# Kernel optimization log

Measured on AMD Instinct MI355X. Metric: run time of the kernel, lower is better.

Reference implementation:

```python
import jax, jax.numpy as jnp
import numpy as np

B, N, H, E, L = 64, 100, 128, 128, 3  # batch, nodes, node_hidden, edge_hidden, gcn layers


def setup_inputs() -> dict:
    key = jax.random.key(0)
    ks = jax.random.split(key, 12)
    s = 0.05
    return dict(
        node=jax.random.normal(ks[0], (B, N, 2), jnp.float32),
        demand=jax.random.uniform(ks[1], (B, N), jnp.float32),
        dis=jax.random.uniform(ks[2], (B, N, N), jnp.float32),
        Wn0=jax.random.normal(ks[3], (3, H), jnp.float32) * s,
        bn0=jnp.zeros((H,), jnp.float32),
        Ws=jax.random.normal(ks[4], (L, H, H), jnp.float32) * s,
        Wngh=jax.random.normal(ks[5], (L, H, H), jnp.float32) * s,
        We=jax.random.normal(ks[6], (E,), jnp.float32) * s,
        be=jnp.zeros((E,), jnp.float32),
        Wih=jax.random.normal(ks[7], (2, H, 3 * H), jnp.float32) * s,
        Whh=jax.random.normal(ks[8], (2, H, 3 * H), jnp.float32) * s,
        bih=jnp.zeros((2, 3 * H), jnp.float32),
        bhh=jnp.zeros((2, 3 * H), jnp.float32),
        Wq=jax.random.normal(ks[9], (H, H), jnp.float32) * s,
        Wc=jax.random.normal(ks[10], (E, 2), jnp.float32) * s,
        bc=jnp.zeros((2,), jnp.float32),
    )


def _gru(xin, h, Wih, Whh, bih, bhh):
    gi = xin @ Wih + bih
    gh = h @ Whh + bhh
    ir, iz, inn = jnp.split(gi, 3, -1)
    hr, hz, hn = jnp.split(gh, 3, -1)
    r = jax.nn.sigmoid(ir + hr)
    z = jax.nn.sigmoid(iz + hz)
    n = jnp.tanh(inn + r * hn)
    return (1.0 - z) * n + z * h


def _decode(x, Wih, Whh, bih, bhh, Wq, sample, key):
    b, n, h = x.shape
    scale = 1.0 / np.sqrt(h).astype(np.float32)

    def step(carry, _):
        last, hid, k = carry
        emb = x[jnp.arange(b), last]                      # [b,h]
        h0 = _gru(emb, hid[0], Wih[0], Whh[0], bih[0], bhh[0])
        h1 = _gru(h0, hid[1], Wih[1], Whh[1], bih[1], bhh[1])
        logits = jnp.einsum('bh,bnh->bn', h1 @ Wq, x) * scale
        logp = jax.nn.log_softmax(logits, -1)
        k, sk = jax.random.split(k)
        if sample:
            ind = jax.random.categorical(sk, logits)
        else:
            ind = jnp.argmax(logits, -1)
        ind = ind.astype(jnp.int32)
        chosen = jnp.take_along_axis(logp, ind[:, None], 1)[:, 0]
        return (ind, jnp.stack([h0, h1]), k), (ind, chosen)

    init = (jnp.zeros((b,), jnp.int32), jnp.zeros((2, b, h), x.dtype), key)
    _, (inds, lps) = jax.lax.scan(step, init, None, length=n - 1)
    solution = jnp.concatenate([jnp.zeros((b, 1), jnp.int32), inds.T], axis=1)  # depot 0 first
    return lps.T, solution  # logprob [b,n-1], solution [b,n]


def _count_dist(sol, dis):
    bidx = jnp.arange(sol.shape[0])[:, None]
    return dis[bidx, sol[:, :-1], sol[:, 1:]].sum(axis=1, keepdims=True)  # [b,1]


def reference(node, demand, dis, Wn0, bn0, Ws, Wngh, We, be, Wih, Whh, bih, bhh, Wq, Wc, bc):
    # --- GCN encoder ---
    h = jax.nn.relu(jnp.concatenate([node, demand[..., None]], -1) @ Wn0 + bn0)  # [B,N,H]
    A = jax.nn.softmax(-dis, -1)  # distance-based soft adjacency
    for l in range(Ws.shape[0]):
        h = jax.nn.relu(h @ Ws[l] + jnp.einsum('bij,bjh->bih', A, h @ Wngh[l]))
    e = jax.nn.relu(dis[..., None] * We + be)  # [B,N,N,E]

    key = jax.random.key(42)
    k1, _ = jax.random.split(key)
    sample_logprob, sample_solution = _decode(h, Wih, Whh, bih, bhh, Wq, True, k1)
    sample_distance = _count_dist(sample_solution, dis)
    _, greedy_solution = _decode(h, Wih, Whh, bih, bhh, Wq, False, k1)
    greedy_distance = _count_dist(greedy_solution, dis)

    predict_matrix = jax.nn.softmax(e @ Wc + bc, -1)  # [B,N,N,2]

    b, n = h.shape[0], h.shape[1]
    bidx = jnp.arange(b)[:, None]
    greedy_solution_matrix = (
        jnp.zeros((b, n, n), jnp.int32)
        .at[bidx, greedy_solution[:, :-1], greedy_solution[:, 1:]]
        .set(1)
    )
    return (sample_logprob, sample_distance, greedy_distance, predict_matrix, greedy_solution_matrix)
```

## Files before the change

### kernel.cpp

```cpp
#include <hip/hip_runtime.h>
#include <math.h>

#define BB 64
#define NN 100
#define HH 128
#define T3 384

#define O0 0
#define O1 6336
#define O2 6400
#define O3 6464
#define O4 1286464

#define TINYF 1.17549435e-38f
#define SCALEF 0.08838834764831845f

__device__ __forceinline__ unsigned rotl32(unsigned x, int d) {
    return (x << d) | (x >> (32 - d));
}

__device__ __forceinline__ void tf2x32(unsigned ks0, unsigned ks1,
                                       unsigned x0, unsigned x1,
                                       unsigned& o0, unsigned& o1) {
    unsigned ks2 = ks0 ^ ks1 ^ 0x1BD11BDAu;
    x0 += ks0; x1 += ks1;
    x0 += x1; x1 = rotl32(x1, 13); x1 ^= x0;
    x0 += x1; x1 = rotl32(x1, 15); x1 ^= x0;
    x0 += x1; x1 = rotl32(x1, 26); x1 ^= x0;
    x0 += x1; x1 = rotl32(x1, 6);  x1 ^= x0;
    x0 += ks1; x1 += ks2 + 1u;
    x0 += x1; x1 = rotl32(x1, 17); x1 ^= x0;
    x0 += x1; x1 = rotl32(x1, 29); x1 ^= x0;
    x0 += x1; x1 = rotl32(x1, 16); x1 ^= x0;
    x0 += x1; x1 = rotl32(x1, 24); x1 ^= x0;
    x0 += ks2; x1 += ks0 + 2u;
    x0 += x1; x1 = rotl32(x1, 13); x1 ^= x0;
    x0 += x1; x1 = rotl32(x1, 15); x1 ^= x0;
    x0 += x1; x1 = rotl32(x1, 26); x1 ^= x0;
    x0 += x1; x1 = rotl32(x1, 6);  x1 ^= x0;
    x0 += ks0; x1 += ks1 + 3u;
    x0 += x1; x1 = rotl32(x1, 17); x1 ^= x0;
    x0 += x1; x1 = rotl32(x1, 29); x1 ^= x0;
    x0 += x1; x1 = rotl32(x1, 16); x1 ^= x0;
    x0 += x1; x1 = rotl32(x1, 24); x1 ^= x0;
    x0 += ks1; x1 += ks2 + 4u;
    x0 += x1; x1 = rotl32(x1, 13); x1 ^= x0;
    x0 += x1; x1 = rotl32(x1, 15); x1 ^= x0;
    x0 += x1; x1 = rotl32(x1, 26); x1 ^= x0;
    x0 += x1; x1 = rotl32(x1, 6);  x1 ^= x0;
    x0 += ks2; x1 += ks0 + 5u;
    o0 = x0; o1 = x1;
}

__device__ __forceinline__ float gumbel_f(unsigned k0, unsigned k1, unsigned f) {
    unsigned o0, o1;
    tf2x32(k0, k1, 0u, f, o0, o1);
    unsigned bits = o0 ^ o1;
    float u01 = __uint_as_float((bits >> 9) | 0x3F800000u) - 1.0f;
    float u = fmaxf(TINYF, u01 * (1.0f - TINYF) + TINYF);
    return -logf(-logf(u));
}

__global__ void k_embed_adj(const float* __restrict__ node, const float* __restrict__ demand,
                            const float* __restrict__ Wn0, const float* __restrict__ bn0,
                            const float* __restrict__ dis,
                            float* __restrict__ h, float* __restrict__ A) {
    int bid = blockIdx.x, tid = threadIdx.x;
    if (bid < 3200) {
        int idx = bid * 256 + tid;
        int r = idx >> 7, c = idx & 127;
        float v = node[r * 2] * Wn0[c] + node[r * 2 + 1] * Wn0[128 + c]
                + demand[r] * Wn0[256 + c] + bn0[c];
        h[idx] = fmaxf(v, 0.0f);
    } else {
        int row = (bid - 3200) * 4 + (tid >> 6);
        int l = tid & 63;
        const float* d = dis + row * NN;
        float v0 = -d[l];
        float v1 = (l + 64 < NN) ? -d[l + 64] : -__builtin_inff();
        float m = fmaxf(v0, v1);
        for (int off = 32; off > 0; off >>= 1) m = fmaxf(m, __shfl_xor(m, off));
        float e0 = expf(v0 - m);
        float e1 = (l + 64 < NN) ? expf(v1 - m) : 0.0f;
        float s = e0 + e1;
        for (int off = 32; off > 0; off >>= 1) s += __shfl_xor(s, off);
        float inv = 1.0f / s;
        A[row * NN + l] = e0 * inv;
        if (l + 64 < NN) A[row * NN + l + 64] = e1 * inv;
    }
}

__global__ void k_hw16(const float* __restrict__ h, const float* __restrict__ W,
                       float* __restrict__ out) {
    __shared__ float hs[16 * 128];
    int block_row = blockIdx.x * 16;
    int tid = threadIdx.x;
    int col = tid & 127;
    int rg = tid >> 7;
    for (int i = tid; i < 16 * 128; i += 256) hs[i] = h[block_row * 128 + i];
    __syncthreads();
    float acc[8] = {0.f, 0.f, 0.f, 0.f, 0.f, 0.f, 0.f, 0.f};
    for (int k = 0; k < 128; k++) {
        float w = W[k * 128 + col];
#pragma unroll
        for (int r = 0; r < 8; r++) acc[r] += hs[(rg + 2 * r) * 128 + k] * w;
    }
#pragma unroll
    for (int r = 0; r < 8; r++)
        out[(block_row + rg + 2 * r) * 128 + col] = acc[r];
}

__global__ void k_zp(const float* __restrict__ h, const float* __restrict__ WqT,
                     const float* __restrict__ Wih, const float* __restrict__ bih,
                     float* __restrict__ Z, float* __restrict__ P0) {
    __shared__ float hs[16 * 128];
    int block_row = blockIdx.x * 16;
    int tid = threadIdx.x;
    int c = tid & 127;
    int rg = tid >> 7;
    int y = blockIdx.y;
    for (int i = tid; i < 16 * 128; i += 256) hs[i] = h[block_row * 128 + i];
    __syncthreads();
    float acc[8] = {0.f, 0.f, 0.f, 0.f, 0.f, 0.f, 0.f, 0.f};
    if (y == 0) {
        for (int k = 0; k < 128; k++) {
            float w = WqT[k * 128 + c];
#pragma unroll
            for (int r = 0; r < 8; r++) acc[r] += hs[(rg + 2 * r) * 128 + k] * w;
        }
#pragma unroll
        for (int r = 0; r < 8; r++)
            Z[(block_row + rg + 2 * r) * 128 + c] = acc[r];
    } else {
        int col = (y - 1) * 128 + c;
        for (int k = 0; k < 128; k++) {
            float w = Wih[k * 384 + col];
#pragma unroll
            for (int r = 0; r < 8; r++) acc[r] += hs[(rg + 2 * r) * 128 + k] * w;
        }
        float bb = bih[col];
#pragma unroll
        for (int r = 0; r < 8; r++)
            P0[(size_t)(block_row + rg + 2 * r) * 384 + col] = acc[r] + bb;
    }
}

__global__ void k_transpose128(const float* __restrict__ Wq, float* __restrict__ WqT) {
    int i = blockIdx.x * 256 + threadIdx.x;
    if (i >= 128 * 128) return;
    int k = i >> 7, c = i & 127;
    WqT[k * 128 + c] = Wq[c * 128 + k];
}

__global__ void k_agg10(const float* __restrict__ h, const float* __restrict__ Ws,
                        const float* __restrict__ A, const float* __restrict__ hw,
                        float* __restrict__ out) {
    __shared__ float hs[10 * 128];
    __shared__ float As[10 * 100];
    int b = blockIdx.x / 10;
    int i0 = (blockIdx.x % 10) * 10;
    int tid = threadIdx.x;
    int col = tid & 127;
    int rg = tid >> 7;
    int rowbase = b * NN + i0;
    for (int i = tid; i < 10 * 128; i += 256) hs[i] = h[rowbase * 128 + i];
    for (int i = tid; i < 10 * 100; i += 256) As[i] = A[rowbase * 100 + i];
    __syncthreads();
    float acc[5] = {0.f, 0.f, 0.f, 0.f, 0.f};
    for (int k = 0; k < 128; k++) {
        float w = Ws[k * 128 + col];
#pragma unroll
        for (int r = 0; r < 5; r++) acc[r] += hs[(rg + 2 * r) * 128 + k] * w;
    }
    const float* hwb = hw + b * NN * 128;
    for (int j = 0; j < NN; j++) {
        float v = hwb[j * 128 + col];
#pragma unroll
        for (int r = 0; r < 5; r++) acc[r] += As[(rg + 2 * r) * 100 + j] * v;
    }
#pragma unroll
    for (int r = 0; r < 5; r++)
        out[(rowbase + rg + 2 * r) * 128 + col] = fmaxf(acc[r], 0.0f);
}

__global__ void k_predict_zero(const float* __restrict__ dis, const float* __restrict__ We,
                               const float* __restrict__ be, const float* __restrict__ Wc,
                               const float* __restrict__ bc, float* __restrict__ out3,
                               float* __restrict__ zp) {
    int bid = blockIdx.x, tid = threadIdx.x;
    if (bid >= 1250) {
        int i = (bid - 1250) * 256 + tid;
        float4 z; z.x = 0.f; z.y = 0.f; z.z = 0.f; z.w = 0.f;
        ((float4*)zp)[i] = z;
        return;
    }
    __shared__ float sWe[128], sbe[128], sc0[128], sc1[128];
    if (tid < 128) {
        sWe[tid] = We[tid];
        sbe[tid] = be[tid];
        sc0[tid] = Wc[tid * 2];
        sc1[tid] = Wc[tid * 2 + 1];
    }
    __syncthreads();
    float b0 = bc[0], b1 = bc[1];
    int p0 = bid * 512 + tid, p1 = p0 + 256;
    float d0 = dis[p0], d1 = dis[p1];
    float a00 = b0, a01 = b1, a10 = b0, a11 = b1;
    for (int k = 0; k < 128; k++) {
        float we = sWe[k], bbe = sbe[k], c0 = sc0[k], c1 = sc1[k];
        float e0 = fmaxf(d0 * we + bbe, 0.0f);
        float e1 = fmaxf(d1 * we + bbe, 0.0f);
        a00 += e0 * c0; a01 += e0 * c1;
        a10 += e1 * c0; a11 += e1 * c1;
    }
    {
        float m = fmaxf(a00, a01);
        float q0 = expf(a00 - m), q1 = expf(a01 - m);
        float inv = 1.0f / (q0 + q1);
        out3[p0 * 2] = q0 * inv;
        out3[p0 * 2 + 1] = q1 * inv;
    }
    {
        float m = fmaxf(a10, a11);
        float q0 = expf(a10 - m), q1 = expf(a11 - m);
        float inv = 1.0f / (q0 + q1);
        out3[p1 * 2] = q0 * inv;
        out3[p1 * 2 + 1] = q1 * inv;
    }
}

__device__ __forceinline__ void matvec_tile4(const float* __restrict__ W,
                                             const float* __restrict__ hp,
                                             int nk4,
                                             float* __restrict__ pg0,
                                             float* __restrict__ pg1) {
    float a00 = 0.f, a01 = 0.f, a02 = 0.f, a03 = 0.f;
    float a10 = 0.f, a11 = 0.f, a12 = 0.f, a13 = 0.f;
#pragma unroll 4
    for (int k4 = 0; k4 < nk4; ++k4) {
        float4 hA = *(const float4*)(hp + 4 * k4);
        float4 hB = *(const float4*)(hp + 132 + 4 * k4);
        const float* Wk = W + (size_t)(4 * k4) * T3;
        float4 w0 = *(const float4*)(Wk);
        float4 w1 = *(const float4*)(Wk + T3);
        float4 w2 = *(const float4*)(Wk + 2 * T3);
        float4 w3 = *(const float4*)(Wk + 3 * T3);
        a00 += hA.x * w0.x; a01 += hA.x * w0.y; a02 += hA.x * w0.z; a03 += hA.x * w0.w;
        a10 += hB.x * w0.x; a11 += hB.x * w0.y; a12 += hB.x * w0.z; a13 += hB.x * w0.w;
        a00 += hA.y * w1.x; a01 += hA.y * w1.y; a02 += hA.y * w1.z; a03 += hA.y * w1.w;
        a10 += hB.y * w1.x; a11 += hB.y * w1.y; a12 += hB.y * w1.z; a13 += hB.y * w1.w;
        a00 += hA.z * w2.x; a01 += hA.z * w2.y; a02 += hA.z * w2.z; a03 += hA.z * w2.w;
        a10 += hB.z * w2.x; a11 += hB.z * w2.y; a12 += hB.z * w2.z; a13 += hB.z * w2.w;
        a00 += hA.w * w3.x; a01 += hA.w * w3.y; a02 += hA.w * w3.z; a03 += hA.w * w3.w;
        a10 += hB.w * w3.x; a11 += hB.w * w3.y; a12 += hB.w * w3.z; a13 += hB.w * w3.w;
    }
    float4 o;
    o.x = a00; o.y = a01; o.z = a02; o.w = a03;
    *(float4*)pg0 = o;
    o.x = a10; o.y = a11; o.z = a12; o.w = a13;
    *(float4*)pg1 = o;
}

__global__ __launch_bounds__(768, 3) void k_decode9(
    const float* __restrict__ P0,
    const float* __restrict__ Z,
    const float* __restrict__ dis,
    const float* __restrict__ Wih,
    const float* __restrict__ Whh,
    const float* __restrict__ bih,
    const float* __restrict__ bhh,
    float* __restrict__ out) {
    __shared__ float Zs[NN * 132];
    __shared__ float h0s[2 * 132], h1s[2 * 132];
    __shared__ float pgA[4 * 2 * 392];
    __shared__ float pgB[4 * 2 * 392];
    __shared__ float pgC[8 * 2 * 392];
    __shared__ float sbhh0[T3], sbih1[T3], sbhh1[T3];
    __shared__ float pl[2 * 2 * 100];
    __shared__ float gum[128];
    __shared__ int s_ind2[2];

    const int tid = threadIdx.x;
    const int b = blockIdx.x;

    const float* __restrict__ Wih1 = Wih + 128 * T3;

    for (int i4 = tid; i4 < NN * 32; i4 += 768) {
        int r = i4 >> 5, c4 = (i4 & 31) * 4;
        *(float4*)&Zs[r * 132 + c4] = *(const float4*)&Z[(b * NN + r) * 128 + c4];
    }
    if (tid < T3) {
        sbhh0[tid] = bhh[tid];
        sbih1[tid] = bih[T3 + tid];
        sbhh1[tid] = bhh[T3 + tid];
    }
    if (tid < 256) {
        int m = tid >> 7, i = tid & 127;
        h0s[m * 132 + i] = 0.0f;
        h1s[m * 132 + i] = 0.0f;
    }
    if (tid == 0) { s_ind2[0] = 0; s_ind2[1] = 0; }

    unsigned kk0, kk1;
    tf2x32(0u, 42u, 0u, 0u, kk0, kk1);

    const int unitA = tid / 384;
    const int rA = tid - unitA * 384;
    const int ksA = rA / 96, j4A = rA - ksA * 96;
    const int j0A = j4A * 4, k0A = ksA * 32;
    const int ksC = tid / 96, j4C = tid - ksC * 96;
    const int j0C = j4C * 4, k0C = ksC * 16;

    int lastm = 0;
    float dist = 0.0f;
    __syncthreads();

    for (int t = 0; t < NN - 1; t++) {
        unsigned sk0, sk1, nkA, nkB;
        tf2x32(kk0, kk1, 0u, 1u, sk0, sk1);
        tf2x32(kk0, kk1, 0u, 0u, nkA, nkB);
        kk0 = nkA; kk1 = nkB;

        float pf_r = 0.f, pf_z = 0.f, pf_n = 0.f;
        if (tid < 256) {
            const float* P0row = P0 + (size_t)(b * NN + s_ind2[tid >> 7]) * T3;
            int i = tid & 127;
            pf_r = P0row[i];
            pf_z = P0row[i + 128];
            pf_n = P0row[i + 256];
        }

        {
            const float* W = Whh + unitA * (128 * T3) + (size_t)k0A * T3 + j0A;
            const float* hp = ((unitA == 0) ? h0s : h1s) + k0A;
            float* pg = (unitA == 0) ? pgA : pgB;
            matvec_tile4(W, hp, 8,
                         &pg[(ksA * 2 + 0) * 392 + j0A],
                         &pg[(ksA * 2 + 1) * 392 + j0A]);
        }
        __syncthreads();

        if (tid < 256) {
            int m = tid >> 7, i = tid & 127;
            float ghr = sbhh0[i], ghz = sbhh0[i + 128], ghn = sbhh0[i + 256];
#pragma unroll
            for (int ks = 0; ks < 4; ks++) {
                int pb = (ks * 2 + m) * 392;
                ghr += pgA[pb + i];
                ghz += pgA[pb + i + 128];
                ghn += pgA[pb + i + 256];
            }
            float rr = 1.0f / (1.0f + expf(-(pf_r + ghr)));
            float zz = 1.0f / (1.0f + expf(-(pf_z + ghz)));
            float nn = tanhf(pf_n + rr * ghn);
            h0s[m * 132 + i] = (1.0f - zz) * nn + zz * h0s[m * 132 + i];
        } else if (tid < 356) {
            int u = tid - 256;
            gum[u] = gumbel_f(sk0, sk1, (unsigned)(b * NN + u));
        }
        __syncthreads();

        {
            const float* W = Wih1 + (size_t)k0C * T3 + j0C;
            matvec_tile4(W, h0s + k0C, 4,
                         &pgC[(ksC * 2 + 0) * 392 + j0C],
                         &pgC[(ksC * 2 + 1) * 392 + j0C]);
        }
        __syncthreads();

        if (tid < 256) {
            int m = tid >> 7, i = tid & 127;
            float gir = sbih1[i], giz = sbih1[i + 128], gin = sbih1[i + 256];
#pragma unroll
            for (int ks = 0; ks < 8; ks++) {
                int pb = (ks * 2 + m) * 392;
                gir += pgC[pb + i];
                giz += pgC[pb + i + 128];
                gin += pgC[pb + i + 256];
            }
            float ghr = sbhh1[i], ghz = sbhh1[i + 128], ghn = sbhh1[i + 256];
#pragma unroll
            for (int ks = 0; ks < 4; ks++) {
                int pb = (ks * 2 + m) * 392;
                ghr += pgB[pb + i];
                ghz += pgB[pb + i + 128];
                ghn += pgB[pb + i + 256];
            }
            float rr = 1.0f / (1.0f + expf(-(gir + ghr)));
            float zz = 1.0f / (1.0f + expf(-(giz + ghz)));
            float nn = tanhf(gin + rr * ghn);
            h1s[m * 132 + i] = (1.0f - zz) * nn + zz * h1s[m * 132 + i];
        }
        __syncthreads();

        if (tid < 200) {
            int ks = tid / 100, n = tid - ks * 100;
            int kk0p = ks * 64;
            const float* Zp = &Zs[n * 132 + kk0p];
            const float* hp = &h1s[kk0p];
            float a0 = 0.f, a1 = 0.f;
#pragma unroll 4
            for (int q = 0; q < 16; q++) {
                float4 z4 = *(const float4*)(Zp + 4 * q);
                float4 hA = *(const float4*)(hp + 4 * q);
                float4 hB = *(const float4*)(hp + 132 + 4 * q);
                a0 += hA.x * z4.x; a0 += hA.y * z4.y; a0 += hA.z * z4.z; a0 += hA.w * z4.w;
                a1 += hB.x * z4.x; a1 += hB.y * z4.y; a1 += hB.z * z4.z; a1 += hB.w * z4.w;
            }
            pl[(0 * 2 + ks) * 100 + n] = a0;
            pl[(1 * 2 + ks) * 100 + n] = a1;
        }
        __syncthreads();

        if (tid < 128) {
            const int m = tid >> 6, lane = tid & 63;
            float v0, v1 = -__builtin_inff();
            v0 = (pl[(m * 2 + 0) * 100 + lane] + pl[(m * 2 + 1) * 100 + lane]) * SCALEF;
            if (lane + 64 < NN)
                v1 = (pl[(m * 2 + 0) * 100 + lane + 64] + pl[(m * 2 + 1) * 100 + lane + 64]) * SCALEF;
            float mx = fmaxf(v0, v1);
            for (int off = 32; off > 0; off >>= 1) mx = fmaxf(mx, __shfl_xor(mx, off));
            float e = expf(v0 - mx) + ((lane + 64 < NN) ? expf(v1 - mx) : 0.0f);
            for (int off = 32; off > 0; off >>= 1) e += __shfl_xor(e, off);
            float a0 = v0, a1 = v1;
            if (m == 0) {
                a0 += gum[lane];
                if (lane + 64 < NN) a1 += gum[lane + 64];
            }
            float bv; int bi;
            if (a1 > a0) { bv = a1; bi = lane + 64; } else { bv = a0; bi = lane; }
            for (int off = 32; off > 0; off >>= 1) {
                float ov = __shfl_xor(bv, off);
                int   oi = __shfl_xor(bi, off);
                if (ov > bv || (ov == bv && oi < bi)) { bv = ov; bi = oi; }
            }
            int ind = bi;
            float la = __shfl(v0, ind & 63);
            float lb = __shfl(v1, ind & 63);
            float lv = (ind < 64) ? la : lb;
            if (lane == 0) {
                if (m == 0) out[O0 + b * (NN - 1) + t] = lv - mx - logf(e);
                else        out[O4 + (size_t)b * NN * NN + lastm * NN + ind] = 1.0f;
                s_ind2[m] = ind;
            }
            dist += dis[b * NN * NN + lastm * NN + ind];
            lastm = ind;
        }
        __syncthreads();
    }

    if (tid == 0)  out[O1 + b] = dist;
    if (tid == 64) out[O2 + b] = dist;
}

extern "C" void kernel_launch(void* const* d_in, const int* in_sizes, int n_in,
                              void* d_out, int out_size, void* d_ws, size_t ws_size,
                              hipStream_t stream) {
    (void)in_sizes; (void)n_in; (void)out_size; (void)ws_size;
    const float* node   = (const float*)d_in[0];
    const float* demand = (const float*)d_in[1];
    const float* dis    = (const float*)d_in[2];
    const float* Wn0    = (const float*)d_in[3];
    const float* bn0    = (const float*)d_in[4];
    const float* Ws     = (const float*)d_in[5];
    const float* Wngh   = (const float*)d_in[6];
    const float* We     = (const float*)d_in[7];
    const float* be     = (const float*)d_in[8];
    const float* Wih    = (const float*)d_in[9];
    const float* Whh    = (const float*)d_in[10];
    const float* bih    = (const float*)d_in[11];
    const float* bhh    = (const float*)d_in[12];
    const float* Wq     = (const float*)d_in[13];
    const float* Wc     = (const float*)d_in[14];
    const float* bc     = (const float*)d_in[15];
    float* out = (float*)d_out;
    float* ws  = (float*)d_ws;

    float* hA  = ws;
    float* hB  = ws + 819200;
    float* hw  = ws + 1638400;
    float* A   = ws + 2457600;
    float* P0  = ws + 2457600;
    float* WqT = ws + 4915200;

    hipLaunchKernelGGL(k_predict_zero, dim3(1875), dim3(256), 0, stream,
                       dis, We, be, Wc, bc, out + O3, out + O4);

    hipLaunchKernelGGL(k_embed_adj, dim3(4800), dim3(256), 0, stream,
                       node, demand, Wn0, bn0, dis, hA, A);

    float* cur = hA;
    float* nxt = hB;
    for (int l = 0; l < 3; l++) {
        hipLaunchKernelGGL(k_hw16, dim3(400), dim3(256), 0, stream, cur, Wngh + l * 16384, hw);
        hipLaunchKernelGGL(k_agg10, dim3(640), dim3(256), 0, stream, cur, Ws + l * 16384, A, hw, nxt);
        float* tswap = cur; cur = nxt; nxt = tswap;
    }

    hipLaunchKernelGGL(k_transpose128, dim3(64), dim3(256), 0, stream, Wq, WqT);
    hipLaunchKernelGGL(k_zp, dim3(400, 4), dim3(256), 0, stream, cur, WqT, Wih, bih, hw, P0);

    hipLaunchKernelGGL(k_decode9, dim3(64), dim3(768), 0, stream,
                       P0, hw, dis, Wih, Whh, bih, bhh, out);
}
```

Baseline: 923.4 us.

## Cache decode GRU input weights in registers, merge preprocessing kernels, vectorize loads

Each decode thread now loads its 16x4 tile of the second-layer GRU input weights into registers once, instead of re-reading it from global memory on every sequential decode step. The predict, zero-fill, embed, adjacency-softmax and Wq transpose kernels are merged into one launch. The small GEMM-like kernels use float4 shared-memory staging and a 4-way unrolled k loop. The extra 64 live floats per thread under a 768-thread, 3-block launch bound may exceed the register budget and spill to scratch.

```diff
diff --git a/kernel.cpp b/kernel.cpp
--- a/kernel.cpp
+++ b/kernel.cpp
@@ -61,10 +61,16 @@
     return -logf(-logf(u));
 }
 
-__global__ void k_embed_adj(const float* __restrict__ node, const float* __restrict__ demand,
-                            const float* __restrict__ Wn0, const float* __restrict__ bn0,
-                            const float* __restrict__ dis,
-                            float* __restrict__ h, float* __restrict__ A) {
+__global__ void k_pre0(const float* __restrict__ node, const float* __restrict__ demand,
+                       const float* __restrict__ Wn0, const float* __restrict__ bn0,
+                       const float* __restrict__ dis,
+                       const float* __restrict__ We, const float* __restrict__ be,
+                       const float* __restrict__ Wc, const float* __restrict__ bc,
+                       const float* __restrict__ Wq,
+                       float* __restrict__ h, float* __restrict__ A,
+                       float* __restrict__ WqT,
+                       float* __restrict__ out3, float* __restrict__ zp) {
+    __shared__ float sWe[128], sbe[128], sc0[128], sc1[128];
     int bid = blockIdx.x, tid = threadIdx.x;
     if (bid < 3200) {
         int idx = bid * 256 + tid;
@@ -72,7 +78,7 @@
         float v = node[r * 2] * Wn0[c] + node[r * 2 + 1] * Wn0[128 + c]
                 + demand[r] * Wn0[256 + c] + bn0[c];
         h[idx] = fmaxf(v, 0.0f);
-    } else {
+    } else if (bid < 4800) {
         int row = (bid - 3200) * 4 + (tid >> 6);
         int l = tid & 63;
         const float* d = dis + row * NN;
@@ -87,6 +93,55 @@
         float inv = 1.0f / s;
         A[row * NN + l] = e0 * inv;
         if (l + 64 < NN) A[row * NN + l + 64] = e1 * inv;
+    } else if (bid < 4864) {
+        int i = (bid - 4800) * 256 + tid;
+        int k = i >> 7, c = i & 127;
+        WqT[k * 128 + c] = Wq[c * 128 + k];
+    } else if (bid < 6114) {
+        if (tid < 128) {
+            sWe[tid] = We[tid];
+            sbe[tid] = be[tid];
+            sc0[tid] = Wc[tid * 2];
+            sc1[tid] = Wc[tid * 2 + 1];
+        }
+        __syncthreads();
+        float b0 = bc[0], b1 = bc[1];
+        int p0 = (bid - 4864) * 512 + tid, p1 = p0 + 256;
+        float d0 = dis[p0], d1 = dis[p1];
+        float a00 = b0, a01 = b1, a10 = b0, a11 = b1;
+        for (int k4 = 0; k4 < 32; k4++) {
+            float4 we = *(const float4*)&sWe[4 * k4];
+            float4 bb = *(const float4*)&sbe[4 * k4];
+            float4 c0 = *(const float4*)&sc0[4 * k4];
+            float4 c1 = *(const float4*)&sc1[4 * k4];
+            float e0, e1;
+            e0 = fmaxf(d0 * we.x + bb.x, 0.0f); a00 += e0 * c0.x; a01 += e0 * c1.x;
+            e1 = fmaxf(d1 * we.x + bb.x, 0.0f); a10 += e1 * c0.x; a11 += e1 * c1.x;
+            e0 = fmaxf(d0 * we.y + bb.y, 0.0f); a00 += e0 * c0.y; a01 += e0 * c1.y;
+            e1 = fmaxf(d1 * we.y + bb.y, 0.0f); a10 += e1 * c0.y; a11 += e1 * c1.y;
+            e0 = fmaxf(d0 * we.z + bb.z, 0.0f); a00 += e0 * c0.z; a01 += e0 * c1.z;
+            e1 = fmaxf(d1 * we.z + bb.z, 0.0f); a10 += e1 * c0.z; a11 += e1 * c1.z;
+            e0 = fmaxf(d0 * we.w + bb.w, 0.0f); a00 += e0 * c0.w; a01 += e0 * c1.w;
+            e1 = fmaxf(d1 * we.w + bb.w, 0.0f); a10 += e1 * c0.w; a11 += e1 * c1.w;
+        }
+        {
+            float m = fmaxf(a00, a01);
+            float q0 = expf(a00 - m), q1 = expf(a01 - m);
+            float inv = 1.0f / (q0 + q1);
+            out3[p0 * 2] = q0 * inv;
+            out3[p0 * 2 + 1] = q1 * inv;
+        }
+        {
+            float m = fmaxf(a10, a11);
+            float q0 = expf(a10 - m), q1 = expf(a11 - m);
+            float inv = 1.0f / (q0 + q1);
+            out3[p1 * 2] = q0 * inv;
+            out3[p1 * 2 + 1] = q1 * inv;
+        }
+    } else {
+        int i = (bid - 6114) * 256 + tid;
+        float4 z; z.x = 0.f; z.y = 0.f; z.z = 0.f; z.w = 0.f;
+        ((float4*)zp)[i] = z;
     }
 }
 
@@ -97,13 +152,20 @@
     int tid = threadIdx.x;
     int col = tid & 127;
     int rg = tid >> 7;
-    for (int i = tid; i < 16 * 128; i += 256) hs[i] = h[block_row * 128 + i];
+    for (int i = tid; i < 16 * 32; i += 256)
+        ((float4*)hs)[i] = ((const float4*)(h + block_row * 128))[i];
     __syncthreads();
     float acc[8] = {0.f, 0.f, 0.f, 0.f, 0.f, 0.f, 0.f, 0.f};
-    for (int k = 0; k < 128; k++) {
-        float w = W[k * 128 + col];
-#pragma unroll
-        for (int r = 0; r < 8; r++) acc[r] += hs[(rg + 2 * r) * 128 + k] * w;
+    for (int k4 = 0; k4 < 32; k4++) {
+        int k = 4 * k4;
+        float w0 = W[k * 128 + col], w1 = W[(k + 1) * 128 + col];
+        float w2 = W[(k + 2) * 128 + col], w3 = W[(k + 3) * 128 + col];
+#pragma unroll
+        for (int r = 0; r < 8; r++) {
+            float4 h4 = *(const float4*)&hs[(rg + 2 * r) * 128 + k];
+            acc[r] += h4.x * w0; acc[r] += h4.y * w1;
+            acc[r] += h4.z * w2; acc[r] += h4.w * w3;
+        }
     }
 #pragma unroll
     for (int r = 0; r < 8; r++)
@@ -119,37 +181,43 @@
     int c = tid & 127;
     int rg = tid >> 7;
     int y = blockIdx.y;
-    for (int i = tid; i < 16 * 128; i += 256) hs[i] = h[block_row * 128 + i];
+    for (int i = tid; i < 16 * 32; i += 256)
+        ((float4*)hs)[i] = ((const float4*)(h + block_row * 128))[i];
     __syncthreads();
     float acc[8] = {0.f, 0.f, 0.f, 0.f, 0.f, 0.f, 0.f, 0.f};
     if (y == 0) {
-        for (int k = 0; k < 128; k++) {
-            float w = WqT[k * 128 + c];
-#pragma unroll
-            for (int r = 0; r < 8; r++) acc[r] += hs[(rg + 2 * r) * 128 + k] * w;
+        for (int k4 = 0; k4 < 32; k4++) {
+            int k = 4 * k4;
+            float w0 = WqT[k * 128 + c], w1 = WqT[(k + 1) * 128 + c];
+            float w2 = WqT[(k + 2) * 128 + c], w3 = WqT[(k + 3) * 128 + c];
+#pragma unroll
+            for (int r = 0; r < 8; r++) {
+                float4 h4 = *(const float4*)&hs[(rg + 2 * r) * 128 + k];
+                acc[r] += h4.x * w0; acc[r] += h4.y * w1;
+                acc[r] += h4.z * w2; acc[r] += h4.w * w3;
+            }
         }
 #pragma unroll
         for (int r = 0; r < 8; r++)
             Z[(block_row + rg + 2 * r) * 128 + c] = acc[r];
     } else {
         int col = (y - 1) * 128 + c;
-        for (int k = 0; k < 128; k++) {
-            float w = Wih[k * 384 + col];
-#pragma unroll
-            for (int r = 0; r < 8; r++) acc[r] += hs[(rg + 2 * r) * 128 + k] * w;
+        for (int k4 = 0; k4 < 32; k4++) {
+            int k = 4 * k4;
+            float w0 = Wih[k * 384 + col], w1 = Wih[(k + 1) * 384 + col];
+            float w2 = Wih[(k + 2) * 384 + col], w3 = Wih[(k + 3) * 384 + col];
+#pragma unroll
+            for (int r = 0; r < 8; r++) {
+                float4 h4 = *(const float4*)&hs[(rg + 2 * r) * 128 + k];
+                acc[r] += h4.x * w0; acc[r] += h4.y * w1;
+                acc[r] += h4.z * w2; acc[r] += h4.w * w3;
+            }
         }
         float bb = bih[col];
 #pragma unroll
         for (int r = 0; r < 8; r++)
             P0[(size_t)(block_row + rg + 2 * r) * 384 + col] = acc[r] + bb;
     }
-}
-
-__global__ void k_transpose128(const float* __restrict__ Wq, float* __restrict__ WqT) {
-    int i = blockIdx.x * 256 + threadIdx.x;
-    if (i >= 128 * 128) return;
-    int k = i >> 7, c = i & 127;
-    WqT[k * 128 + c] = Wq[c * 128 + k];
 }
 
 __global__ void k_agg10(const float* __restrict__ h, const float* __restrict__ Ws,
@@ -163,70 +231,38 @@
     int col = tid & 127;
     int rg = tid >> 7;
     int rowbase = b * NN + i0;
-    for (int i = tid; i < 10 * 128; i += 256) hs[i] = h[rowbase * 128 + i];
-    for (int i = tid; i < 10 * 100; i += 256) As[i] = A[rowbase * 100 + i];
+    for (int i = tid; i < 10 * 32; i += 256)
+        ((float4*)hs)[i] = ((const float4*)(h + rowbase * 128))[i];
+    for (int i = tid; i < 10 * 25; i += 256)
+        ((float4*)As)[i] = ((const float4*)(A + rowbase * 100))[i];
     __syncthreads();
     float acc[5] = {0.f, 0.f, 0.f, 0.f, 0.f};
-    for (int k = 0; k < 128; k++) {
-        float w = Ws[k * 128 + col];
-#pragma unroll
-        for (int r = 0; r < 5; r++) acc[r] += hs[(rg + 2 * r) * 128 + k] * w;
+    for (int k4 = 0; k4 < 32; k4++) {
+        int k = 4 * k4;
+        float w0 = Ws[k * 128 + col], w1 = Ws[(k + 1) * 128 + col];
+        float w2 = Ws[(k + 2) * 128 + col], w3 = Ws[(k + 3) * 128 + col];
+#pragma unroll
+        for (int r = 0; r < 5; r++) {
+            float4 h4 = *(const float4*)&hs[(rg + 2 * r) * 128 + k];
+            acc[r] += h4.x * w0; acc[r] += h4.y * w1;
+            acc[r] += h4.z * w2; acc[r] += h4.w * w3;
+        }
     }
     const float* hwb = hw + b * NN * 128;
-    for (int j = 0; j < NN; j++) {
-        float v = hwb[j * 128 + col];
-#pragma unroll
-        for (int r = 0; r < 5; r++) acc[r] += As[(rg + 2 * r) * 100 + j] * v;
+    for (int j4 = 0; j4 < 25; j4++) {
+        int j = 4 * j4;
+        float v0 = hwb[j * 128 + col], v1 = hwb[(j + 1) * 128 + col];
+        float v2 = hwb[(j + 2) * 128 + col], v3 = hwb[(j + 3) * 128 + col];
+#pragma unroll
+        for (int r = 0; r < 5; r++) {
+            float4 a4 = *(const float4*)&As[(rg + 2 * r) * 100 + j];
+            acc[r] += a4.x * v0; acc[r] += a4.y * v1;
+            acc[r] += a4.z * v2; acc[r] += a4.w * v3;
+        }
     }
 #pragma unroll
     for (int r = 0; r < 5; r++)
         out[(rowbase + rg + 2 * r) * 128 + col] = fmaxf(acc[r], 0.0f);
-}
-
-__global__ void k_predict_zero(const float* __restrict__ dis, const float* __restrict__ We,
-                               const float* __restrict__ be, const float* __restrict__ Wc,
-                               const float* __restrict__ bc, float* __restrict__ out3,
-                               float* __restrict__ zp) {
-    int bid = blockIdx.x, tid = threadIdx.x;
-    if (bid >= 1250) {
-        int i = (bid - 1250) * 256 + tid;
-        float4 z; z.x = 0.f; z.y = 0.f; z.z = 0.f; z.w = 0.f;
-        ((float4*)zp)[i] = z;
-        return;
-    }
-    __shared__ float sWe[128], sbe[128], sc0[128], sc1[128];
-    if (tid < 128) {
-        sWe[tid] = We[tid];
-        sbe[tid] = be[tid];
-        sc0[tid] = Wc[tid * 2];
-        sc1[tid] = Wc[tid * 2 + 1];
-    }
-    __syncthreads();
-    float b0 = bc[0], b1 = bc[1];
-    int p0 = bid * 512 + tid, p1 = p0 + 256;
-    float d0 = dis[p0], d1 = dis[p1];
-    float a00 = b0, a01 = b1, a10 = b0, a11 = b1;
-    for (int k = 0; k < 128; k++) {
-        float we = sWe[k], bbe = sbe[k], c0 = sc0[k], c1 = sc1[k];
-        float e0 = fmaxf(d0 * we + bbe, 0.0f);
-        float e1 = fmaxf(d1 * we + bbe, 0.0f);
-        a00 += e0 * c0; a01 += e0 * c1;
-        a10 += e1 * c0; a11 += e1 * c1;
-    }
-    {
-        float m = fmaxf(a00, a01);
-        float q0 = expf(a00 - m), q1 = expf(a01 - m);
-        float inv = 1.0f / (q0 + q1);
-        out3[p0 * 2] = q0 * inv;
-        out3[p0 * 2 + 1] = q1 * inv;
-    }
-    {
-        float m = fmaxf(a10, a11);
-        float q0 = expf(a10 - m), q1 = expf(a11 - m);
-        float inv = 1.0f / (q0 + q1);
-        out3[p1 * 2] = q0 * inv;
-        out3[p1 * 2 + 1] = q1 * inv;
-    }
 }
 
 __device__ __forceinline__ void matvec_tile4(const float* __restrict__ W,
@@ -261,7 +297,7 @@
     *(float4*)pg1 = o;
 }
 
-__global__ __launch_bounds__(768, 3) void k_decode9(
+__global__ __launch_bounds__(768, 3) void k_decode10(
     const float* __restrict__ P0,
     const float* __restrict__ Z,
     const float* __restrict__ dis,
@@ -285,31 +321,39 @@
 
     const float* __restrict__ Wih1 = Wih + 128 * T3;
 
-    for (int i4 = tid; i4 < NN * 32; i4 += 768) {
-        int r = i4 >> 5, c4 = (i4 & 31) * 4;
-        *(float4*)&Zs[r * 132 + c4] = *(const float4*)&Z[(b * NN + r) * 128 + c4];
-    }
-    if (tid < T3) {
-        sbhh0[tid] = bhh[tid];
-        sbih1[tid] = bih[T3 + tid];
-        sbhh1[tid] = bhh[T3 + tid];
-    }
-    if (tid < 256) {
-        int m = tid >> 7, i = tid & 127;
-        h0s[m * 132 + i] = 0.0f;
-        h1s[m * 132 + i] = 0.0f;
-    }
-    if (tid == 0) { s_ind2[0] = 0; s_ind2[1] = 0; }
-
-    unsigned kk0, kk1;
-    tf2x32(0u, 42u, 0u, 0u, kk0, kk1);
-
     const int unitA = tid / 384;
     const int rA = tid - unitA * 384;
     const int ksA = rA / 96, j4A = rA - ksA * 96;
     const int j0A = j4A * 4, k0A = ksA * 32;
     const int ksC = tid / 96, j4C = tid - ksC * 96;
     const int j0C = j4C * 4, k0C = ksC * 16;
+
+    float4 pw[16];
+    {
+        const float* Wc = Wih1 + (size_t)k0C * T3 + j0C;
+#pragma unroll
+        for (int k = 0; k < 16; k++)
+            pw[k] = *(const float4*)(Wc + (size_t)k * T3);
+    }
+
+    for (int i4 = tid; i4 < NN * 32; i4 += 768) {
+        int r = i4 >> 5, c4 = (i4 & 31) * 4;
+        *(float4*)&Zs[r * 132 + c4] = *(const float4*)&Z[(b * NN + r) * 128 + c4];
+    }
+    if (tid < T3) {
+        sbhh0[tid] = bhh[tid];
+        sbih1[tid] = bih[T3 + tid];
+        sbhh1[tid] = bhh[T3 + tid];
+    }
+    if (tid < 256) {
+        int m = tid >> 7, i = tid & 127;
+        h0s[m * 132 + i] = 0.0f;
+        h1s[m * 132 + i] = 0.0f;
+    }
+    if (tid == 0) { s_ind2[0] = 0; s_ind2[1] = 0; }
+
+    unsigned kk0, kk1;
+    tf2x32(0u, 42u, 0u, 0u, kk0, kk1);
 
     int lastm = 0;
     float dist = 0.0f;
@@ -361,10 +405,31 @@
         __syncthreads();
 
         {
-            const float* W = Wih1 + (size_t)k0C * T3 + j0C;
-            matvec_tile4(W, h0s + k0C, 4,
-                         &pgC[(ksC * 2 + 0) * 392 + j0C],
-                         &pgC[(ksC * 2 + 1) * 392 + j0C]);
+            const float* hp = h0s + k0C;
+            float a00 = 0.f, a01 = 0.f, a02 = 0.f, a03 = 0.f;
+            float a10 = 0.f, a11 = 0.f, a12 = 0.f, a13 = 0.f;
+#pragma unroll
+            for (int k4 = 0; k4 < 4; ++k4) {
+                float4 hA = *(const float4*)(hp + 4 * k4);
+                float4 hB = *(const float4*)(hp + 132 + 4 * k4);
+                float4 w0 = pw[4 * k4 + 0];
+                float4 w1 = pw[4 * k4 + 1];
+                float4 w2 = pw[4 * k4 + 2];
+                float4 w3 = pw[4 * k4 + 3];
+                a00 += hA.x * w0.x; a01 += hA.x * w0.y; a02 += hA.x * w0.z; a03 += hA.x * w0.w;
+                a10 += hB.x * w0.x; a11 += hB.x * w0.y; a12 += hB.x * w0.z; a13 += hB.x * w0.w;
+                a00 += hA.y * w1.x; a01 += hA.y * w1.y; a02 += hA.y * w1.z; a03 += hA.y * w1.w;
+                a10 += hB.y * w1.x; a11 += hB.y * w1.y; a12 += hB.y * w1.z; a13 += hB.y * w1.w;
+                a00 += hA.z * w2.x; a01 += hA.z * w2.y; a02 += hA.z * w2.z; a03 += hA.z * w2.w;
+                a10 += hB.z * w2.x; a11 += hB.z * w2.y; a12 += hB.z * w2.z; a13 += hB.z * w2.w;
+                a00 += hA.w * w3.x; a01 += hA.w * w3.y; a02 += hA.w * w3.z; a03 += hA.w * w3.w;
+                a10 += hB.w * w3.x; a11 += hB.w * w3.y; a12 += hB.w * w3.z; a13 += hB.w * w3.w;
+            }
+            float4 o;
+            o.x = a00; o.y = a01; o.z = a02; o.w = a03;
+            *(float4*)&pgC[(ksC * 2 + 0) * 392 + j0C] = o;
+            o.x = a10; o.y = a11; o.z = a12; o.w = a13;
+            *(float4*)&pgC[(ksC * 2 + 1) * 392 + j0C] = o;
         }
         __syncthreads();
 
@@ -483,11 +548,9 @@
     float* P0  = ws + 2457600;
     float* WqT = ws + 4915200;
 
-    hipLaunchKernelGGL(k_predict_zero, dim3(1875), dim3(256), 0, stream,
-                       dis, We, be, Wc, bc, out + O3, out + O4);
-
-    hipLaunchKernelGGL(k_embed_adj, dim3(4800), dim3(256), 0, stream,
-                       node, demand, Wn0, bn0, dis, hA, A);
+    hipLaunchKernelGGL(k_pre0, dim3(6739), dim3(256), 0, stream,
+                       node, demand, Wn0, bn0, dis, We, be, Wc, bc, Wq,
+                       hA, A, WqT, out + O3, out + O4);
 
     float* cur = hA;
     float* nxt = hB;
@@ -497,9 +560,8 @@
         float* tswap = cur; cur = nxt; nxt = tswap;
     }
 
-    hipLaunchKernelGGL(k_transpose128, dim3(64), dim3(256), 0, stream, Wq, WqT);
     hipLaunchKernelGGL(k_zp, dim3(400, 4), dim3(256), 0, stream, cur, WqT, Wih, bih, hw, P0);
 
-    hipLaunchKernelGGL(k_decode9, dim3(64), dim3(768), 0, stream,
+    hipLaunchKernelGGL(k_decode10, dim3(64), dim3(768), 0, stream,
                        P0, hw, dis, Wih, Whh, bih, bhh, out);
 }
```

Measured after the change: 911.0 us. Within noise of the previous version (-1.3%).
